# Kernel optimization log

Hardware: AMD Instinct MI355X
Metric: run time of the kernel (lower is better)

Reference implementation:

```python
import jax, jax.numpy as jnp
import numpy as np

N_NODES = 100000


def _gcn_norm(src, dst, n_nodes, n_edges):
    # PyG gcn_norm with add_self_loops=False: deg over target (col) index
    ones = jnp.ones((n_edges,), dtype=jnp.float32)
    deg = jax.ops.segment_sum(ones, dst, num_segments=n_nodes)
    dinv = jnp.where(deg > 0, jax.lax.rsqrt(deg), 0.0)
    return dinv[src] * dinv[dst]  # [E]


def _arma_conv(x, src, dst, ew, init_w, root_w, bias, n_nodes):
    # x: [N, Fin]; init_w/root_w: [K, Fin, Fout]; bias: [K, 1, Fout]
    h = jnp.einsum('nf,kfo->kno', x, init_w)          # [K, N, Fout]
    msg = h[:, src, :] * ew[None, :, None]             # [K, E, Fout]
    agg = jax.vmap(lambda m: jax.ops.segment_sum(m, dst, num_segments=n_nodes))(msg)
    out = agg + jnp.einsum('nf,kfo->kno', x, root_w) + bias
    return jax.nn.relu(out).mean(axis=0)               # mean over stacks K


def setup_inputs() -> dict:
    key = jax.random.key(0)
    ks = jax.random.split(key, 8)
    n, e = N_NODES, 3200000
    nfeat, hid, nclass, K = 512, 16, 40, 2
    x = jax.random.normal(ks[0], (n, nfeat), dtype=jnp.float32)
    edge_index = jax.random.randint(ks[1], (2, e), 0, n, dtype=jnp.int32)
    s1 = (1.0 / np.sqrt(nfeat)).astype(np.float32) if isinstance(np.sqrt(nfeat), np.ndarray) else np.float32(1.0 / np.sqrt(nfeat))
    s2 = np.float32(1.0 / np.sqrt(hid))
    iw1 = jax.random.normal(ks[2], (K, nfeat, hid), dtype=jnp.float32) * s1
    rw1 = jax.random.normal(ks[3], (K, nfeat, hid), dtype=jnp.float32) * s1
    b1 = jax.random.normal(ks[4], (K, 1, hid), dtype=jnp.float32) * 0.01
    iw2 = jax.random.normal(ks[5], (K, hid, nclass), dtype=jnp.float32) * s2
    rw2 = jax.random.normal(ks[6], (K, hid, nclass), dtype=jnp.float32) * s2
    b2 = jax.random.normal(ks[7], (K, 1, nclass), dtype=jnp.float32) * 0.01
    return {'x': x, 'edge_index': edge_index, 'iw1': iw1, 'rw1': rw1, 'b1': b1,
            'iw2': iw2, 'rw2': rw2, 'b2': b2}


def reference(x, edge_index, iw1, rw1, b1, iw2, rw2, b2):
    src, dst = edge_index[0], edge_index[1]
    n = N_NODES
    ew = _gcn_norm(src, dst, n, src.shape[0])
    h = _arma_conv(x, src, dst, ew, iw1, rw1, b1, n)   # [N, 16]
    out = _arma_conv(h, src, dst, ew, iw2, rw2, b2, n) # [N, nclass]
    return out
```

## Files before the change

### kernel.cpp

```cpp
#include <hip/hip_runtime.h>


#define TB 256
#define CHA 4096

typedef __attribute__((ext_vector_type(8))) short bf8;
typedef __attribute__((ext_vector_type(4))) float f4;

__device__ inline unsigned short f2bf_rne(float f) {
  unsigned int u = __float_as_uint(f);
  unsigned int r = u + 0x7fffu + ((u >> 16) & 1u);
  return (unsigned short)(r >> 16);
}
__device__ inline float bf2f(unsigned short h) {
  return __uint_as_float(((unsigned int)h) << 16);
}
__device__ inline float bflo(unsigned int u) { return __uint_as_float(u << 16); }
__device__ inline float bfhi(unsigned int u) { return __uint_as_float(u & 0xffff0000u); }
__device__ inline unsigned int bfpack(float lo, float hi) {
  return (unsigned int)f2bf_rne(lo) | ((unsigned int)f2bf_rne(hi) << 16);
}

#define ACC8(v)                                   \
  do {                                            \
    a[0] += bflo((v).x); a[1] += bfhi((v).x);     \
    a[2] += bflo((v).y); a[3] += bfhi((v).y);     \
    a[4] += bflo((v).z); a[5] += bfhi((v).z);     \
    a[6] += bflo((v).w); a[7] += bfhi((v).w);     \
  } while (0)

#define ACC4(v)                                   \
  do {                                            \
    a[0] += bflo((v).x); a[1] += bfhi((v).x);     \
    a[2] += bflo((v).y); a[3] += bfhi((v).y);     \
  } while (0)

__global__ __launch_bounds__(TB) void k_countA(const int* __restrict__ dst,
                                               int* __restrict__ ccnt, int E) {
  __shared__ int cnt[256];
  int tid = threadIdx.x;
  cnt[tid] = 0;
  __syncthreads();
  int e0 = blockIdx.x * CHA;
  int e1 = min(e0 + CHA, E);
  for (int e = e0 + tid; e < e1; e += TB) atomicAdd(&cnt[dst[e] >> 9], 1);
  __syncthreads();
  if (cnt[tid] > 0) atomicAdd(&ccnt[tid], cnt[tid]);
}

__global__ __launch_bounds__(256) void k_scanC(const int* __restrict__ ccnt,
                                               int* __restrict__ cbase,
                                               int* __restrict__ ccur) {
  __shared__ int sh[256];
  int tid = threadIdx.x;
  int v = ccnt[tid];
  sh[tid] = v;
  __syncthreads();
  for (int d = 1; d < 256; d <<= 1) {
    int t = (tid >= d) ? sh[tid - d] : 0;
    __syncthreads();
    sh[tid] += t;
    __syncthreads();
  }
  int excl = sh[tid] - v;
  cbase[tid] = excl;
  ccur[tid] = excl;
  if (tid == 255) cbase[256] = sh[255];
}

__global__ __launch_bounds__(TB) void k_binA(const int* __restrict__ src,
                                             const int* __restrict__ dst,
                                             int* __restrict__ ccur,
                                             unsigned int* __restrict__ epairs,
                                             int E) {
  __shared__ int cnt[256];
  __shared__ int gb[256];
  int tid = threadIdx.x;
  cnt[tid] = 0;
  __syncthreads();
  int e0 = blockIdx.x * CHA;
  int e1 = min(e0 + CHA, E);
  for (int e = e0 + tid; e < e1; e += TB) atomicAdd(&cnt[dst[e] >> 9], 1);
  __syncthreads();
  int c = cnt[tid];
  if (c > 0) gb[tid] = atomicAdd(&ccur[tid], c);
  __syncthreads();
  cnt[tid] = 0;
  __syncthreads();
  for (int e = e0 + tid; e < e1; e += TB) {
    int dv = dst[e];
    int b = dv >> 9;
    int r = atomicAdd(&cnt[b], 1);
    epairs[gb[b] + r] = ((unsigned int)src[e] << 9) | (unsigned int)(dv & 511);
  }
}

__global__ __launch_bounds__(TB) void k_binB(const unsigned int* __restrict__ epairs,
                                             const int* __restrict__ cbase,
                                             int* __restrict__ degi,
                                             int* __restrict__ offsets,
                                             int* __restrict__ srcs,
                                             float* __restrict__ dinv, int N) {
  __shared__ int cnt[512];
  __shared__ int pre[512];
  int b = blockIdx.x;
  int n0 = b << 9;
  int tid = threadIdx.x;
  int beg = cbase[b], end = cbase[b + 1];
  int i0 = tid, i1 = tid + 256;
  cnt[i0] = 0; cnt[i1] = 0;
  __syncthreads();
  for (int e = beg + tid; e < end; e += TB)
    atomicAdd(&cnt[epairs[e] & 511u], 1);
  __syncthreads();
  pre[i0] = cnt[i0]; pre[i1] = cnt[i1];
  __syncthreads();
  for (int d = 1; d < 512; d <<= 1) {
    int t0 = (i0 >= d) ? pre[i0 - d] : 0;
    int t1 = (i1 >= d) ? pre[i1 - d] : 0;
    __syncthreads();
    pre[i0] += t0; pre[i1] += t1;
    __syncthreads();
  }
  int e0 = pre[i0] - cnt[i0];
  int e1x = pre[i1] - cnt[i1];
  if (n0 + i0 < N) {
    int c0 = cnt[i0];
    degi[n0 + i0] = c0;
    offsets[n0 + i0] = beg + e0;
    dinv[n0 + i0] = c0 > 0 ? rsqrtf((float)c0) : 0.0f;
  }
  if (n0 + i1 < N) {
    int c1 = cnt[i1];
    degi[n0 + i1] = c1;
    offsets[n0 + i1] = beg + e1x;
    dinv[n0 + i1] = c1 > 0 ? rsqrtf((float)c1) : 0.0f;
  }
  __syncthreads();
  cnt[i0] = e0; cnt[i1] = e1x;
  __syncthreads();
  for (int e = beg + tid; e < end; e += TB) {
    unsigned int p = epairs[e];
    int pos = atomicAdd(&cnt[p & 511u], 1);
    srcs[beg + pos] = (int)(p >> 9);
  }
}

__global__ __launch_bounds__(TB) void k_wsplit(const float* __restrict__ iw1,
                                               const float* __restrict__ rw1,
                                               short* __restrict__ Whi,
                                               short* __restrict__ Wlo) {
  int idx = blockIdx.x * TB + threadIdx.x;
  if (idx >= 32768) return;
  int j = idx & 7;
  int l = (idx >> 3) & 63;
  int t = (idx >> 9) & 3;
  int c = idx >> 11;
  int k = c * 32 + (l >> 4) * 8 + j;
  int n = t * 16 + (l & 15);
  float w;
  if (n < 16)
    w = iw1[k * 16 + n];
  else if (n < 32)
    w = iw1[8192 + k * 16 + (n - 16)];
  else if (n < 48)
    w = rw1[k * 16 + (n - 32)];
  else
    w = rw1[8192 + k * 16 + (n - 48)];
  unsigned short h = f2bf_rne(w);
  float res = w - bf2f(h);
  Whi[idx] = (short)h;
  Wlo[idx] = (short)f2bf_rne(res);
}

__global__ __launch_bounds__(TB) void k_gemm1_mfma(const float* __restrict__ x,
                                                   const short* __restrict__ Whi,
                                                   const short* __restrict__ Wlo,
                                                   const float* __restrict__ dinv,
                                                   unsigned short* __restrict__ Hs,
                                                   float* __restrict__ R, int N) {
  int lane = threadIdx.x & 63;
  int wave = threadIdx.x >> 6;
  int row0 = blockIdx.x * 64 + wave * 16;
  int m = lane & 15, quad = lane >> 4;
  int r = row0 + m;
  bool rv = (r < N);
  const float* xr = x + (size_t)r * 512;

  f4 acc[4];
#pragma unroll
  for (int t = 0; t < 4; t++) acc[t] = (f4){0.f, 0.f, 0.f, 0.f};

  for (int c = 0; c < 16; ++c) {
    float xv[8];
    if (rv) {
      f4 a0 = *(const f4*)(xr + c * 32 + quad * 8);
      f4 a1 = *(const f4*)(xr + c * 32 + quad * 8 + 4);
      xv[0] = a0.x; xv[1] = a0.y; xv[2] = a0.z; xv[3] = a0.w;
      xv[4] = a1.x; xv[5] = a1.y; xv[6] = a1.z; xv[7] = a1.w;
    } else {
#pragma unroll
      for (int j = 0; j < 8; ++j) xv[j] = 0.f;
    }
    bf8 ahi, alo;
#pragma unroll
    for (int j = 0; j < 8; ++j) {
      unsigned short h = f2bf_rne(xv[j]);
      float res = xv[j] - bf2f(h);
      ahi[j] = (short)h;
      alo[j] = (short)f2bf_rne(res);
    }
    const short* wb = Whi + ((size_t)(c * 4) * 64 + lane) * 8;
    const short* wl = Wlo + ((size_t)(c * 4) * 64 + lane) * 8;
#pragma unroll
    for (int t = 0; t < 4; ++t) {
      bf8 bh = *(const bf8*)(wb + t * 512);
      bf8 bl = *(const bf8*)(wl + t * 512);
      acc[t] = __builtin_amdgcn_mfma_f32_16x16x32_bf16(ahi, bh, acc[t], 0, 0, 0);
      acc[t] = __builtin_amdgcn_mfma_f32_16x16x32_bf16(alo, bh, acc[t], 0, 0, 0);
      acc[t] = __builtin_amdgcn_mfma_f32_16x16x32_bf16(ahi, bl, acc[t], 0, 0, 0);
    }
  }
  float dv[4];
#pragma unroll
  for (int g = 0; g < 4; ++g) {
    int ro = row0 + quad * 4 + g;
    dv[g] = (ro < N) ? dinv[ro] : 0.f;
  }
#pragma unroll
  for (int t = 0; t < 4; ++t) {
#pragma unroll
    for (int g = 0; g < 4; ++g) {
      int ro = row0 + quad * 4 + g;
      if (ro < N) {
        if (t < 2)
          Hs[(size_t)ro * 32 + t * 16 + m] = f2bf_rne(acc[t][g] * dv[g]);
        else
          R[(size_t)ro * 32 + (t - 2) * 16 + m] = acc[t][g];
      }
    }
  }
}

__global__ __launch_bounds__(TB) void k_prop1(const int* __restrict__ offsets,
                                              const int* __restrict__ degi,
                                              const int* __restrict__ srcs,
                                              const unsigned short* __restrict__ Hs,
                                              const float* __restrict__ R,
                                              const float* __restrict__ dinv,
                                              const float* __restrict__ b1,
                                              float* __restrict__ h,
                                              unsigned short* __restrict__ hs, int N) {
  int tid = blockIdx.x * TB + threadIdx.x;
  int q = tid & 3;
  int n = tid >> 2;
  if (n >= N) return;
  int beg = offsets[n], cnt = degi[n];
  const unsigned short* Hq = Hs + q * 8;
  float a[8];
#pragma unroll
  for (int j = 0; j < 8; j++) a[j] = 0.f;

  int i = 0;
  if (cnt >= 4) {
    int s0 = srcs[beg], s1 = srcs[beg + 1], s2 = srcs[beg + 2], s3 = srcs[beg + 3];
    for (; i + 8 <= cnt; i += 4) {
      uint4 v0 = *(const uint4*)(Hq + (size_t)s0 * 32);
      uint4 v1 = *(const uint4*)(Hq + (size_t)s1 * 32);
      uint4 v2 = *(const uint4*)(Hq + (size_t)s2 * 32);
      uint4 v3 = *(const uint4*)(Hq + (size_t)s3 * 32);
      s0 = srcs[beg + i + 4]; s1 = srcs[beg + i + 5];
      s2 = srcs[beg + i + 6]; s3 = srcs[beg + i + 7];
      ACC8(v0); ACC8(v1); ACC8(v2); ACC8(v3);
    }
    {
      uint4 v0 = *(const uint4*)(Hq + (size_t)s0 * 32);
      uint4 v1 = *(const uint4*)(Hq + (size_t)s1 * 32);
      uint4 v2 = *(const uint4*)(Hq + (size_t)s2 * 32);
      uint4 v3 = *(const uint4*)(Hq + (size_t)s3 * 32);
      ACC8(v0); ACC8(v1); ACC8(v2); ACC8(v3);
      i += 4;
    }
  }
  for (; i < cnt; ++i) {
    int s = srcs[beg + i];
    uint4 v = *(const uint4*)(Hq + (size_t)s * 32);
    ACC8(v);
  }

  float dvn = dinv[n];
  f4 r0 = *(const f4*)(R + (size_t)n * 32 + q * 8);
  f4 r1 = *(const f4*)(R + (size_t)n * 32 + q * 8 + 4);
  float rr[8] = {r0.x, r0.y, r0.z, r0.w, r1.x, r1.y, r1.z, r1.w};
  float vv[8];
#pragma unroll
  for (int j = 0; j < 8; j++) {
    int f = q * 8 + j;
    vv[j] = fmaxf(a[j] * dvn + rr[j] + b1[(f >> 4) * 16 + (f & 15)], 0.f);
  }
  float pv[8];
#pragma unroll
  for (int j = 0; j < 8; j++) pv[j] = __shfl_xor(vv[j], 2);
  if (q < 2) {
    float hv[8];
#pragma unroll
    for (int j = 0; j < 8; j++) hv[j] = 0.5f * (vv[j] + pv[j]);
    f4 o0 = {hv[0], hv[1], hv[2], hv[3]};
    f4 o1 = {hv[4], hv[5], hv[6], hv[7]};
    *(f4*)(h + (size_t)n * 16 + q * 8) = o0;
    *(f4*)(h + (size_t)n * 16 + q * 8 + 4) = o1;
    uint4 ob;
    ob.x = bfpack(hv[0] * dvn, hv[1] * dvn);
    ob.y = bfpack(hv[2] * dvn, hv[3] * dvn);
    ob.z = bfpack(hv[4] * dvn, hv[5] * dvn);
    ob.w = bfpack(hv[6] * dvn, hv[7] * dvn);
    *(uint4*)(hs + (size_t)n * 16 + q * 8) = ob;
  }
}

__global__ __launch_bounds__(TB) void k_prop2(const int* __restrict__ offsets,
                                              const int* __restrict__ degi,
                                              const int* __restrict__ srcs,
                                              const unsigned short* __restrict__ hs,
                                              const float* __restrict__ dinv,
                                              float* __restrict__ Ah, int N) {
  int tid = blockIdx.x * TB + threadIdx.x;
  int q = tid & 3;
  int n = tid >> 2;
  if (n >= N) return;
  int beg = offsets[n], cnt = degi[n];
  const unsigned short* Hq = hs + q * 4;
  float a[4] = {0.f, 0.f, 0.f, 0.f};

  int i = 0;
  if (cnt >= 4) {
    int s0 = srcs[beg], s1 = srcs[beg + 1], s2 = srcs[beg + 2], s3 = srcs[beg + 3];
    for (; i + 8 <= cnt; i += 4) {
      uint2 v0 = *(const uint2*)(Hq + (size_t)s0 * 16);
      uint2 v1 = *(const uint2*)(Hq + (size_t)s1 * 16);
      uint2 v2 = *(const uint2*)(Hq + (size_t)s2 * 16);
      uint2 v3 = *(const uint2*)(Hq + (size_t)s3 * 16);
      s0 = srcs[beg + i + 4]; s1 = srcs[beg + i + 5];
      s2 = srcs[beg + i + 6]; s3 = srcs[beg + i + 7];
      ACC4(v0); ACC4(v1); ACC4(v2); ACC4(v3);
    }
    {
      uint2 v0 = *(const uint2*)(Hq + (size_t)s0 * 16);
      uint2 v1 = *(const uint2*)(Hq + (size_t)s1 * 16);
      uint2 v2 = *(const uint2*)(Hq + (size_t)s2 * 16);
      uint2 v3 = *(const uint2*)(Hq + (size_t)s3 * 16);
      ACC4(v0); ACC4(v1); ACC4(v2); ACC4(v3);
      i += 4;
    }
  }
  for (; i < cnt; ++i) {
    int s = srcs[beg + i];
    uint2 v = *(const uint2*)(Hq + (size_t)s * 16);
    ACC4(v);
  }

  float dvn = dinv[n];
  f4 o = {a[0] * dvn, a[1] * dvn, a[2] * dvn, a[3] * dvn};
  *(f4*)(Ah + (size_t)n * 16 + q * 4) = o;
}

__global__ __launch_bounds__(TB) void k_final(const float* __restrict__ Ah,
                                              const float* __restrict__ h,
                                              const float* __restrict__ iw2,
                                              const float* __restrict__ rw2,
                                              const float* __restrict__ b2,
                                              float* __restrict__ out, int N) {
  __shared__ float w_iw[2 * 16 * 40];
  __shared__ float w_rw[2 * 16 * 40];
  __shared__ float w_b[2 * 40];
  for (int i = threadIdx.x; i < 1280; i += TB) {
    w_iw[i] = iw2[i];
    w_rw[i] = rw2[i];
  }
  for (int i = threadIdx.x; i < 80; i += TB) w_b[i] = b2[i];
  __syncthreads();

  int idx = blockIdx.x * TB + threadIdx.x;
  if (idx >= N * 40) return;
  int n = idx / 40;
  int o = idx - n * 40;
  float a[16], hr[16];
#pragma unroll
  for (int f = 0; f < 16; f++) {
    a[f] = Ah[(size_t)n * 16 + f];
    hr[f] = h[(size_t)n * 16 + f];
  }
  float res = 0.f;
#pragma unroll
  for (int k = 0; k < 2; k++) {
    float s = w_b[k * 40 + o];
#pragma unroll
    for (int f = 0; f < 16; f++) {
      s += a[f] * w_iw[(k * 16 + f) * 40 + o];
      s += hr[f] * w_rw[(k * 16 + f) * 40 + o];
    }
    res += fmaxf(s, 0.f);
  }
  out[idx] = 0.5f * res;
}

extern "C" void kernel_launch(void* const* d_in, const int* in_sizes, int n_in,
                              void* d_out, int out_size, void* d_ws, size_t ws_size,
                              hipStream_t stream) {
  const float* x = (const float*)d_in[0];
  const int* ei = (const int*)d_in[1];
  const float* iw1 = (const float*)d_in[2];
  const float* rw1 = (const float*)d_in[3];
  const float* b1 = (const float*)d_in[4];
  const float* iw2 = (const float*)d_in[5];
  const float* rw2 = (const float*)d_in[6];
  const float* b2 = (const float*)d_in[7];
  float* out = (float*)d_out;

  const int N = in_sizes[0] / 512;
  const int E = in_sizes[1] / 2;
  const int* src = ei;
  const int* dst = ei + E;
  const int NC = (N + 511) >> 9;

  char* base = (char*)d_ws;
  size_t off = 0;
  auto alloc = [&](size_t bytes) -> void* {
    off = (off + 255) & ~(size_t)255;
    void* p = base + off;
    off += bytes;
    return p;
  };
  int* degi = (int*)alloc((size_t)N * 4);
  float* dinv = (float*)alloc((size_t)N * 4);
  int* offsets = (int*)alloc((size_t)N * 4);
  int* ccnt = (int*)alloc(260 * 4);
  int* cbase = (int*)alloc(260 * 4);
  int* ccur = (int*)alloc(260 * 4);
  size_t epair_bytes = (size_t)E * 4;
  size_t r_bytes = (size_t)N * 32 * 4;
  unsigned int* epairs =
      (unsigned int*)alloc(epair_bytes > r_bytes ? epair_bytes : r_bytes);
  int* srcs = (int*)alloc((size_t)E * 4);
  unsigned short* Hs = (unsigned short*)alloc((size_t)N * 32 * 2);
  float* hbuf = (float*)alloc((size_t)N * 16 * 4);
  unsigned short* hs = (unsigned short*)alloc((size_t)N * 16 * 2);
  float* Ah = (float*)alloc((size_t)N * 16 * 4);
  short* Whi = (short*)alloc(32768 * 2);
  short* Wlo = (short*)alloc(32768 * 2);
  float* R = (float*)epairs;
  (void)ws_size;

  hipMemsetAsync(ccnt, 0, 260 * 4, stream);

  int NBLK = (E + CHA - 1) / CHA;
  k_countA<<<NBLK, TB, 0, stream>>>(dst, ccnt, E);
  k_scanC<<<1, 256, 0, stream>>>(ccnt, cbase, ccur);
  k_binA<<<NBLK, TB, 0, stream>>>(src, dst, ccur, epairs, E);
  k_binB<<<NC, TB, 0, stream>>>(epairs, cbase, degi, offsets, srcs, dinv, N);
  k_wsplit<<<128, TB, 0, stream>>>(iw1, rw1, Whi, Wlo);
  k_gemm1_mfma<<<(N + 63) / 64, TB, 0, stream>>>(x, Whi, Wlo, dinv, Hs, R, N);
  k_prop1<<<((size_t)N * 4 + TB - 1) / TB, TB, 0, stream>>>(offsets, degi, srcs, Hs, R,
                                                            dinv, b1, hbuf, hs, N);
  k_prop2<<<((size_t)N * 4 + TB - 1) / TB, TB, 0, stream>>>(offsets, degi, srcs, hs,
                                                            dinv, Ah, N);
  k_final<<<((size_t)N * 40 + TB - 1) / TB, TB, 0, stream>>>(Ah, hbuf, iw2, rw2, b2, out, N);
}
```

Measured before the change: 565.9 us.

## Pad CSR rows to multiples of four and degree-sort nodes for propagation

Each node's CSR neighbor list is padded to a multiple of four entries. The padding points at a zeroed dummy row N, which lets both propagation kernels drop their scalar tail loop. A degree histogram, scan and scatter build a permutation so that threads in a wavefront handle nodes of similar degree, which is meant to reduce divergence in the gather loops. The cost is three extra small kernels, extra padded srcs storage, an indirection through perm, and scattered output writes in prop1 and prop2.

```diff
diff --git a/kernel.cpp b/kernel.cpp
--- a/kernel.cpp
+++ b/kernel.cpp
@@ -3,6 +3,7 @@
 
 #define TB 256
 #define CHA 4096
+#define PADB 1536
 
 typedef __attribute__((ext_vector_type(8))) short bf8;
 typedef __attribute__((ext_vector_type(4))) float f4;
@@ -107,13 +108,16 @@
   int n0 = b << 9;
   int tid = threadIdx.x;
   int beg = cbase[b], end = cbase[b + 1];
+  int pbase = beg + b * PADB;
   int i0 = tid, i1 = tid + 256;
   cnt[i0] = 0; cnt[i1] = 0;
   __syncthreads();
   for (int e = beg + tid; e < end; e += TB)
     atomicAdd(&cnt[epairs[e] & 511u], 1);
   __syncthreads();
-  pre[i0] = cnt[i0]; pre[i1] = cnt[i1];
+  int pd0 = (cnt[i0] + 3) & ~3;
+  int pd1 = (cnt[i1] + 3) & ~3;
+  pre[i0] = pd0; pre[i1] = pd1;
   __syncthreads();
   for (int d = 1; d < 512; d <<= 1) {
     int t0 = (i0 >= d) ? pre[i0 - d] : 0;
@@ -122,36 +126,68 @@
     pre[i0] += t0; pre[i1] += t1;
     __syncthreads();
   }
-  int e0 = pre[i0] - cnt[i0];
-  int e1x = pre[i1] - cnt[i1];
+  int s0 = pre[i0] - pd0;
+  int s1 = pre[i1] - pd1;
   if (n0 + i0 < N) {
     int c0 = cnt[i0];
     degi[n0 + i0] = c0;
-    offsets[n0 + i0] = beg + e0;
+    offsets[n0 + i0] = pbase + s0;
     dinv[n0 + i0] = c0 > 0 ? rsqrtf((float)c0) : 0.0f;
   }
   if (n0 + i1 < N) {
     int c1 = cnt[i1];
     degi[n0 + i1] = c1;
-    offsets[n0 + i1] = beg + e1x;
+    offsets[n0 + i1] = pbase + s1;
     dinv[n0 + i1] = c1 > 0 ? rsqrtf((float)c1) : 0.0f;
   }
   __syncthreads();
-  cnt[i0] = e0; cnt[i1] = e1x;
+  cnt[i0] = s0; cnt[i1] = s1;
   __syncthreads();
   for (int e = beg + tid; e < end; e += TB) {
     unsigned int p = epairs[e];
     int pos = atomicAdd(&cnt[p & 511u], 1);
-    srcs[beg + pos] = (int)(p >> 9);
-  }
+    srcs[pbase + pos] = (int)(p >> 9);
+  }
+  __syncthreads();
+  for (int j = cnt[i0]; j < pre[i0]; ++j) srcs[pbase + j] = N;
+  for (int j = cnt[i1]; j < pre[i1]; ++j) srcs[pbase + j] = N;
+}
+
+__global__ __launch_bounds__(TB) void k_dhist(const int* __restrict__ degi,
+                                              int* __restrict__ dhist, int N) {
+  __shared__ int cnt[256];
+  cnt[threadIdx.x] = 0;
+  __syncthreads();
+  int n = blockIdx.x * TB + threadIdx.x;
+  if (n < N) {
+    int bin = min((degi[n] + 3) >> 2, 255);
+    atomicAdd(&cnt[bin], 1);
+  }
+  __syncthreads();
+  if (cnt[threadIdx.x] > 0) atomicAdd(&dhist[threadIdx.x], cnt[threadIdx.x]);
+}
+
+__global__ __launch_bounds__(TB) void k_dscatter(const int* __restrict__ degi,
+                                                 int* __restrict__ dcur,
+                                                 int* __restrict__ perm, int N) {
+  int n = blockIdx.x * TB + threadIdx.x;
+  if (n >= N) return;
+  int bin = min((degi[n] + 3) >> 2, 255);
+  int pos = atomicAdd(&dcur[bin], 1);
+  perm[pos] = n;
 }
 
 __global__ __launch_bounds__(TB) void k_wsplit(const float* __restrict__ iw1,
                                                const float* __restrict__ rw1,
                                                short* __restrict__ Whi,
-                                               short* __restrict__ Wlo) {
+                                               short* __restrict__ Wlo,
+                                               unsigned short* __restrict__ Hs,
+                                               unsigned short* __restrict__ hs,
+                                               int N) {
   int idx = blockIdx.x * TB + threadIdx.x;
   if (idx >= 32768) return;
+  if (idx < 32) Hs[(size_t)N * 32 + idx] = 0;
+  if (idx < 16) hs[(size_t)N * 16 + idx] = 0;
   int j = idx & 7;
   int l = (idx >> 3) & 63;
   int t = (idx >> 9) & 3;
@@ -242,7 +278,8 @@
   }
 }
 
-__global__ __launch_bounds__(TB) void k_prop1(const int* __restrict__ offsets,
+__global__ __launch_bounds__(TB) void k_prop1(const int* __restrict__ perm,
+                                              const int* __restrict__ offsets,
                                               const int* __restrict__ degi,
                                               const int* __restrict__ srcs,
                                               const unsigned short* __restrict__ Hs,
@@ -253,18 +290,20 @@
                                               unsigned short* __restrict__ hs, int N) {
   int tid = blockIdx.x * TB + threadIdx.x;
   int q = tid & 3;
-  int n = tid >> 2;
-  if (n >= N) return;
+  int idx = tid >> 2;
+  if (idx >= N) return;
+  int n = perm[idx];
   int beg = offsets[n], cnt = degi[n];
+  int pdeg = (cnt + 3) & ~3;
   const unsigned short* Hq = Hs + q * 8;
   float a[8];
 #pragma unroll
   for (int j = 0; j < 8; j++) a[j] = 0.f;
 
-  int i = 0;
-  if (cnt >= 4) {
+  if (pdeg) {
     int s0 = srcs[beg], s1 = srcs[beg + 1], s2 = srcs[beg + 2], s3 = srcs[beg + 3];
-    for (; i + 8 <= cnt; i += 4) {
+    int i = 0;
+    for (; i + 8 <= pdeg; i += 4) {
       uint4 v0 = *(const uint4*)(Hq + (size_t)s0 * 32);
       uint4 v1 = *(const uint4*)(Hq + (size_t)s1 * 32);
       uint4 v2 = *(const uint4*)(Hq + (size_t)s2 * 32);
@@ -279,13 +318,7 @@
       uint4 v2 = *(const uint4*)(Hq + (size_t)s2 * 32);
       uint4 v3 = *(const uint4*)(Hq + (size_t)s3 * 32);
       ACC8(v0); ACC8(v1); ACC8(v2); ACC8(v3);
-      i += 4;
-    }
-  }
-  for (; i < cnt; ++i) {
-    int s = srcs[beg + i];
-    uint4 v = *(const uint4*)(Hq + (size_t)s * 32);
-    ACC8(v);
+    }
   }
 
   float dvn = dinv[n];
@@ -296,7 +329,7 @@
 #pragma unroll
   for (int j = 0; j < 8; j++) {
     int f = q * 8 + j;
-    vv[j] = fmaxf(a[j] * dvn + rr[j] + b1[(f >> 4) * 16 + (f & 15)], 0.f);
+    vv[j] = fmaxf(a[j] * dvn + rr[j] + b1[f], 0.f);
   }
   float pv[8];
 #pragma unroll
@@ -318,7 +351,8 @@
   }
 }
 
-__global__ __launch_bounds__(TB) void k_prop2(const int* __restrict__ offsets,
+__global__ __launch_bounds__(TB) void k_prop2(const int* __restrict__ perm,
+                                              const int* __restrict__ offsets,
                                               const int* __restrict__ degi,
                                               const int* __restrict__ srcs,
                                               const unsigned short* __restrict__ hs,
@@ -326,16 +360,18 @@
                                               float* __restrict__ Ah, int N) {
   int tid = blockIdx.x * TB + threadIdx.x;
   int q = tid & 3;
-  int n = tid >> 2;
-  if (n >= N) return;
+  int idx = tid >> 2;
+  if (idx >= N) return;
+  int n = perm[idx];
   int beg = offsets[n], cnt = degi[n];
+  int pdeg = (cnt + 3) & ~3;
   const unsigned short* Hq = hs + q * 4;
   float a[4] = {0.f, 0.f, 0.f, 0.f};
 
-  int i = 0;
-  if (cnt >= 4) {
+  if (pdeg) {
     int s0 = srcs[beg], s1 = srcs[beg + 1], s2 = srcs[beg + 2], s3 = srcs[beg + 3];
-    for (; i + 8 <= cnt; i += 4) {
+    int i = 0;
+    for (; i + 8 <= pdeg; i += 4) {
       uint2 v0 = *(const uint2*)(Hq + (size_t)s0 * 16);
       uint2 v1 = *(const uint2*)(Hq + (size_t)s1 * 16);
       uint2 v2 = *(const uint2*)(Hq + (size_t)s2 * 16);
@@ -350,13 +386,7 @@
       uint2 v2 = *(const uint2*)(Hq + (size_t)s2 * 16);
       uint2 v3 = *(const uint2*)(Hq + (size_t)s3 * 16);
       ACC4(v0); ACC4(v1); ACC4(v2); ACC4(v3);
-      i += 4;
-    }
-  }
-  for (; i < cnt; ++i) {
-    int s = srcs[beg + i];
-    uint2 v = *(const uint2*)(Hq + (size_t)s * 16);
-    ACC4(v);
+    }
   }
 
   float dvn = dinv[n];
@@ -434,35 +464,44 @@
   int* degi = (int*)alloc((size_t)N * 4);
   float* dinv = (float*)alloc((size_t)N * 4);
   int* offsets = (int*)alloc((size_t)N * 4);
-  int* ccnt = (int*)alloc(260 * 4);
+  int* perm = (int*)alloc((size_t)N * 4);
+  int* cz = (int*)alloc(1040 * 4);
+  int* ccnt = cz;
+  int* dhist = cz + 260;
   int* cbase = (int*)alloc(260 * 4);
   int* ccur = (int*)alloc(260 * 4);
+  int* dbase = (int*)alloc(260 * 4);
+  int* dcur = (int*)alloc(260 * 4);
   size_t epair_bytes = (size_t)E * 4;
   size_t r_bytes = (size_t)N * 32 * 4;
   unsigned int* epairs =
       (unsigned int*)alloc(epair_bytes > r_bytes ? epair_bytes : r_bytes);
-  int* srcs = (int*)alloc((size_t)E * 4);
-  unsigned short* Hs = (unsigned short*)alloc((size_t)N * 32 * 2);
+  int* srcs = (int*)alloc(((size_t)E + 256 * PADB) * 4);
+  unsigned short* Hs = (unsigned short*)alloc((size_t)(N + 1) * 32 * 2);
   float* hbuf = (float*)alloc((size_t)N * 16 * 4);
-  unsigned short* hs = (unsigned short*)alloc((size_t)N * 16 * 2);
+  unsigned short* hs = (unsigned short*)alloc((size_t)(N + 1) * 16 * 2);
   float* Ah = (float*)alloc((size_t)N * 16 * 4);
   short* Whi = (short*)alloc(32768 * 2);
   short* Wlo = (short*)alloc(32768 * 2);
   float* R = (float*)epairs;
   (void)ws_size;
 
-  hipMemsetAsync(ccnt, 0, 260 * 4, stream);
+  hipMemsetAsync(cz, 0, 1040 * 4, stream);
 
   int NBLK = (E + CHA - 1) / CHA;
+  int NNB = (N + TB - 1) / TB;
   k_countA<<<NBLK, TB, 0, stream>>>(dst, ccnt, E);
   k_scanC<<<1, 256, 0, stream>>>(ccnt, cbase, ccur);
   k_binA<<<NBLK, TB, 0, stream>>>(src, dst, ccur, epairs, E);
   k_binB<<<NC, TB, 0, stream>>>(epairs, cbase, degi, offsets, srcs, dinv, N);
-  k_wsplit<<<128, TB, 0, stream>>>(iw1, rw1, Whi, Wlo);
+  k_dhist<<<NNB, TB, 0, stream>>>(degi, dhist, N);
+  k_scanC<<<1, 256, 0, stream>>>(dhist, dbase, dcur);
+  k_dscatter<<<NNB, TB, 0, stream>>>(degi, dcur, perm, N);
+  k_wsplit<<<128, TB, 0, stream>>>(iw1, rw1, Whi, Wlo, Hs, hs, N);
   k_gemm1_mfma<<<(N + 63) / 64, TB, 0, stream>>>(x, Whi, Wlo, dinv, Hs, R, N);
-  k_prop1<<<((size_t)N * 4 + TB - 1) / TB, TB, 0, stream>>>(offsets, degi, srcs, Hs, R,
-                                                            dinv, b1, hbuf, hs, N);
-  k_prop2<<<((size_t)N * 4 + TB - 1) / TB, TB, 0, stream>>>(offsets, degi, srcs, hs,
-                                                            dinv, Ah, N);
+  k_prop1<<<((size_t)N * 4 + TB - 1) / TB, TB, 0, stream>>>(perm, offsets, degi, srcs,
+                                                            Hs, R, dinv, b1, hbuf, hs, N);
+  k_prop2<<<((size_t)N * 4 + TB - 1) / TB, TB, 0, stream>>>(perm, offsets, degi, srcs,
+                                                            hs, dinv, Ah, N);
   k_final<<<((size_t)N * 40 + TB - 1) / TB, TB, 0, stream>>>(Ah, hbuf, iw2, rw2, b2, out, N);
 }
```

Result: slower. 1.059 ms (+87.2%).

## Build CSR via global atomic ranks and pad rows to multiples of four

Applied to the files above, without the earlier changes.

Replaces the two-level bucketed binning (count, scan, bin by chunk, then per-bucket sort) with a per-edge global atomicAdd on degree that records each edge's rank, a three-kernel prefix scan over nodes, and a direct scatter of sources into CSR slots. Each node's edge list is padded to a multiple of four, with the padding pointing at a zeroed sentinel row, so the propagation kernels can drop their scalar tail loops. The cost is contended global atomics on 3.2M edges, extra rank storage and scattered writes, plus dummy gathers for the padding slots. The b1 indexing is also simplified to an equivalent form.

```diff
diff --git a/kernel.cpp b/kernel.cpp
--- a/kernel.cpp
+++ b/kernel.cpp
@@ -2,7 +2,6 @@
 
 
 #define TB 256
-#define CHA 4096
 
 typedef __attribute__((ext_vector_type(8))) short bf8;
 typedef __attribute__((ext_vector_type(4))) float f4;
@@ -35,123 +34,90 @@
     a[2] += bflo((v).y); a[3] += bfhi((v).y);     \
   } while (0)
 
-__global__ __launch_bounds__(TB) void k_countA(const int* __restrict__ dst,
-                                               int* __restrict__ ccnt, int E) {
-  __shared__ int cnt[256];
-  int tid = threadIdx.x;
-  cnt[tid] = 0;
+__global__ __launch_bounds__(TB) void k_deg(const int* __restrict__ dst,
+                                            int* __restrict__ degi,
+                                            int* __restrict__ rank, int E) {
+  int e = blockIdx.x * TB + threadIdx.x;
+  if (e >= E) return;
+  int d = dst[e];
+  rank[e] = atomicAdd(&degi[d], 1);
+}
+
+__global__ __launch_bounds__(TB) void k_scan1(const int* __restrict__ degi,
+                                              int* __restrict__ offsets,
+                                              int* __restrict__ bsum,
+                                              float* __restrict__ dinv, int N) {
+  __shared__ int sh[TB];
+  int t = threadIdx.x;
+  int n = blockIdx.x * TB + t;
+  int d = (n < N) ? degi[n] : 0;
+  int pd = (d + 3) & ~3;
+  sh[t] = pd;
   __syncthreads();
-  int e0 = blockIdx.x * CHA;
-  int e1 = min(e0 + CHA, E);
-  for (int e = e0 + tid; e < e1; e += TB) atomicAdd(&cnt[dst[e] >> 9], 1);
+  for (int o = 1; o < TB; o <<= 1) {
+    int v = (t >= o) ? sh[t - o] : 0;
+    __syncthreads();
+    sh[t] += v;
+    __syncthreads();
+  }
+  if (n < N) {
+    offsets[n] = sh[t] - pd;
+    dinv[n] = d > 0 ? rsqrtf((float)d) : 0.0f;
+  }
+  if (t == TB - 1) bsum[blockIdx.x] = sh[t];
+}
+
+__global__ __launch_bounds__(512) void k_scan2(const int* __restrict__ bsum,
+                                               int* __restrict__ bbase, int NB) {
+  __shared__ int sh[512];
+  int t = threadIdx.x;
+  int v = (t < NB) ? bsum[t] : 0;
+  sh[t] = v;
   __syncthreads();
-  if (cnt[tid] > 0) atomicAdd(&ccnt[tid], cnt[tid]);
-}
-
-__global__ __launch_bounds__(256) void k_scanC(const int* __restrict__ ccnt,
-                                               int* __restrict__ cbase,
-                                               int* __restrict__ ccur) {
-  __shared__ int sh[256];
-  int tid = threadIdx.x;
-  int v = ccnt[tid];
-  sh[tid] = v;
-  __syncthreads();
-  for (int d = 1; d < 256; d <<= 1) {
-    int t = (tid >= d) ? sh[tid - d] : 0;
+  for (int o = 1; o < 512; o <<= 1) {
+    int x = (t >= o) ? sh[t - o] : 0;
     __syncthreads();
-    sh[tid] += t;
+    sh[t] += x;
     __syncthreads();
   }
-  int excl = sh[tid] - v;
-  cbase[tid] = excl;
-  ccur[tid] = excl;
-  if (tid == 255) cbase[256] = sh[255];
-}
-
-__global__ __launch_bounds__(TB) void k_binA(const int* __restrict__ src,
-                                             const int* __restrict__ dst,
-                                             int* __restrict__ ccur,
-                                             unsigned int* __restrict__ epairs,
-                                             int E) {
-  __shared__ int cnt[256];
-  __shared__ int gb[256];
-  int tid = threadIdx.x;
-  cnt[tid] = 0;
-  __syncthreads();
-  int e0 = blockIdx.x * CHA;
-  int e1 = min(e0 + CHA, E);
-  for (int e = e0 + tid; e < e1; e += TB) atomicAdd(&cnt[dst[e] >> 9], 1);
-  __syncthreads();
-  int c = cnt[tid];
-  if (c > 0) gb[tid] = atomicAdd(&ccur[tid], c);
-  __syncthreads();
-  cnt[tid] = 0;
-  __syncthreads();
-  for (int e = e0 + tid; e < e1; e += TB) {
-    int dv = dst[e];
-    int b = dv >> 9;
-    int r = atomicAdd(&cnt[b], 1);
-    epairs[gb[b] + r] = ((unsigned int)src[e] << 9) | (unsigned int)(dv & 511);
-  }
-}
-
-__global__ __launch_bounds__(TB) void k_binB(const unsigned int* __restrict__ epairs,
-                                             const int* __restrict__ cbase,
-                                             int* __restrict__ degi,
-                                             int* __restrict__ offsets,
-                                             int* __restrict__ srcs,
-                                             float* __restrict__ dinv, int N) {
-  __shared__ int cnt[512];
-  __shared__ int pre[512];
-  int b = blockIdx.x;
-  int n0 = b << 9;
-  int tid = threadIdx.x;
-  int beg = cbase[b], end = cbase[b + 1];
-  int i0 = tid, i1 = tid + 256;
-  cnt[i0] = 0; cnt[i1] = 0;
-  __syncthreads();
-  for (int e = beg + tid; e < end; e += TB)
-    atomicAdd(&cnt[epairs[e] & 511u], 1);
-  __syncthreads();
-  pre[i0] = cnt[i0]; pre[i1] = cnt[i1];
-  __syncthreads();
-  for (int d = 1; d < 512; d <<= 1) {
-    int t0 = (i0 >= d) ? pre[i0 - d] : 0;
-    int t1 = (i1 >= d) ? pre[i1 - d] : 0;
-    __syncthreads();
-    pre[i0] += t0; pre[i1] += t1;
-    __syncthreads();
-  }
-  int e0 = pre[i0] - cnt[i0];
-  int e1x = pre[i1] - cnt[i1];
-  if (n0 + i0 < N) {
-    int c0 = cnt[i0];
-    degi[n0 + i0] = c0;
-    offsets[n0 + i0] = beg + e0;
-    dinv[n0 + i0] = c0 > 0 ? rsqrtf((float)c0) : 0.0f;
-  }
-  if (n0 + i1 < N) {
-    int c1 = cnt[i1];
-    degi[n0 + i1] = c1;
-    offsets[n0 + i1] = beg + e1x;
-    dinv[n0 + i1] = c1 > 0 ? rsqrtf((float)c1) : 0.0f;
-  }
-  __syncthreads();
-  cnt[i0] = e0; cnt[i1] = e1x;
-  __syncthreads();
-  for (int e = beg + tid; e < end; e += TB) {
-    unsigned int p = epairs[e];
-    int pos = atomicAdd(&cnt[p & 511u], 1);
-    srcs[beg + pos] = (int)(p >> 9);
-  }
+  if (t < NB) bbase[t] = sh[t] - v;
+}
+
+__global__ __launch_bounds__(TB) void k_scan3(const int* __restrict__ degi,
+                                              int* __restrict__ offsets,
+                                              const int* __restrict__ bbase,
+                                              int* __restrict__ srcs, int N) {
+  int n = blockIdx.x * TB + threadIdx.x;
+  if (n >= N) return;
+  int off = offsets[n] + bbase[n >> 8];
+  offsets[n] = off;
+  int d = degi[n];
+  int pd = (d + 3) & ~3;
+  for (int j = d; j < pd; ++j) srcs[off + j] = N;
+}
+
+__global__ __launch_bounds__(TB) void k_scatter(const int* __restrict__ src,
+                                                const int* __restrict__ dst,
+                                                const int* __restrict__ rank,
+                                                const int* __restrict__ offsets,
+                                                int* __restrict__ srcs, int E) {
+  int e = blockIdx.x * TB + threadIdx.x;
+  if (e >= E) return;
+  int d = dst[e];
+  srcs[offsets[d] + rank[e]] = src[e];
 }
 
 __global__ __launch_bounds__(TB) void k_wsplit(const float* __restrict__ iw1,
                                                const float* __restrict__ rw1,
                                                short* __restrict__ Whi,
-                                               short* __restrict__ Wlo) {
+                                               short* __restrict__ Wlo,
+                                               unsigned short* __restrict__ Hs,
+                                               unsigned short* __restrict__ hs,
+                                               int N) {
   int idx = blockIdx.x * TB + threadIdx.x;
   if (idx >= 32768) return;
+  if (idx < 32) Hs[(size_t)N * 32 + idx] = 0;
+  if (idx < 16) hs[(size_t)N * 16 + idx] = 0;
   int j = idx & 7;
   int l = (idx >> 3) & 63;
   int t = (idx >> 9) & 3;
@@ -256,15 +222,16 @@
   int n = tid >> 2;
   if (n >= N) return;
   int beg = offsets[n], cnt = degi[n];
+  int pdeg = (cnt + 3) & ~3;
   const unsigned short* Hq = Hs + q * 8;
   float a[8];
 #pragma unroll
   for (int j = 0; j < 8; j++) a[j] = 0.f;
 
-  int i = 0;
-  if (cnt >= 4) {
+  if (pdeg) {
     int s0 = srcs[beg], s1 = srcs[beg + 1], s2 = srcs[beg + 2], s3 = srcs[beg + 3];
-    for (; i + 8 <= cnt; i += 4) {
+    int i = 0;
+    for (; i + 8 <= pdeg; i += 4) {
       uint4 v0 = *(const uint4*)(Hq + (size_t)s0 * 32);
       uint4 v1 = *(const uint4*)(Hq + (size_t)s1 * 32);
       uint4 v2 = *(const uint4*)(Hq + (size_t)s2 * 32);
@@ -279,13 +246,7 @@
       uint4 v2 = *(const uint4*)(Hq + (size_t)s2 * 32);
       uint4 v3 = *(const uint4*)(Hq + (size_t)s3 * 32);
       ACC8(v0); ACC8(v1); ACC8(v2); ACC8(v3);
-      i += 4;
-    }
-  }
-  for (; i < cnt; ++i) {
-    int s = srcs[beg + i];
-    uint4 v = *(const uint4*)(Hq + (size_t)s * 32);
-    ACC8(v);
+    }
   }
 
   float dvn = dinv[n];
@@ -296,7 +257,7 @@
 #pragma unroll
   for (int j = 0; j < 8; j++) {
     int f = q * 8 + j;
-    vv[j] = fmaxf(a[j] * dvn + rr[j] + b1[(f >> 4) * 16 + (f & 15)], 0.f);
+    vv[j] = fmaxf(a[j] * dvn + rr[j] + b1[f], 0.f);
   }
   float pv[8];
 #pragma unroll
@@ -329,13 +290,14 @@
   int n = tid >> 2;
   if (n >= N) return;
   int beg = offsets[n], cnt = degi[n];
+  int pdeg = (cnt + 3) & ~3;
   const unsigned short* Hq = hs + q * 4;
   float a[4] = {0.f, 0.f, 0.f, 0.f};
 
-  int i = 0;
-  if (cnt >= 4) {
+  if (pdeg) {
     int s0 = srcs[beg], s1 = srcs[beg + 1], s2 = srcs[beg + 2], s3 = srcs[beg + 3];
-    for (; i + 8 <= cnt; i += 4) {
+    int i = 0;
+    for (; i + 8 <= pdeg; i += 4) {
       uint2 v0 = *(const uint2*)(Hq + (size_t)s0 * 16);
       uint2 v1 = *(const uint2*)(Hq + (size_t)s1 * 16);
       uint2 v2 = *(const uint2*)(Hq + (size_t)s2 * 16);
@@ -350,13 +312,7 @@
       uint2 v2 = *(const uint2*)(Hq + (size_t)s2 * 16);
       uint2 v3 = *(const uint2*)(Hq + (size_t)s3 * 16);
       ACC4(v0); ACC4(v1); ACC4(v2); ACC4(v3);
-      i += 4;
-    }
-  }
-  for (; i < cnt; ++i) {
-    int s = srcs[beg + i];
-    uint2 v = *(const uint2*)(Hq + (size_t)s * 16);
-    ACC4(v);
+    }
   }
 
   float dvn = dinv[n];
@@ -421,7 +377,6 @@
   const int E = in_sizes[1] / 2;
   const int* src = ei;
   const int* dst = ei + E;
-  const int NC = (N + 511) >> 9;
 
   char* base = (char*)d_ws;
   size_t off = 0;
@@ -434,35 +389,34 @@
   int* degi = (int*)alloc((size_t)N * 4);
   float* dinv = (float*)alloc((size_t)N * 4);
   int* offsets = (int*)alloc((size_t)N * 4);
-  int* ccnt = (int*)alloc(260 * 4);
-  int* cbase = (int*)alloc(260 * 4);
-  int* ccur = (int*)alloc(260 * 4);
-  size_t epair_bytes = (size_t)E * 4;
+  int* bsum = (int*)alloc(512 * 4);
+  int* bbase = (int*)alloc(512 * 4);
+  size_t rank_bytes = (size_t)E * 4;
   size_t r_bytes = (size_t)N * 32 * 4;
-  unsigned int* epairs =
-      (unsigned int*)alloc(epair_bytes > r_bytes ? epair_bytes : r_bytes);
-  int* srcs = (int*)alloc((size_t)E * 4);
-  unsigned short* Hs = (unsigned short*)alloc((size_t)N * 32 * 2);
+  int* rank = (int*)alloc(rank_bytes > r_bytes ? rank_bytes : r_bytes);
+  int* srcs = (int*)alloc(((size_t)E + 4 * (size_t)N) * 4);
+  unsigned short* Hs = (unsigned short*)alloc((size_t)(N + 1) * 32 * 2);
   float* hbuf = (float*)alloc((size_t)N * 16 * 4);
-  unsigned short* hs = (unsigned short*)alloc((size_t)N * 16 * 2);
+  unsigned short* hs = (unsigned short*)alloc((size_t)(N + 1) * 16 * 2);
   float* Ah = (float*)alloc((size_t)N * 16 * 4);
   short* Whi = (short*)alloc(32768 * 2);
   short* Wlo = (short*)alloc(32768 * 2);
-  float* R = (float*)epairs;
+  float* R = (float*)rank;
   (void)ws_size;
 
-  hipMemsetAsync(ccnt, 0, 260 * 4, stream);
-
-  int NBLK = (E + CHA - 1) / CHA;
-  k_countA<<<NBLK, TB, 0, stream>>>(dst, ccnt, E);
-  k_scanC<<<1, 256, 0, stream>>>(ccnt, cbase, ccur);
-  k_binA<<<NBLK, TB, 0, stream>>>(src, dst, ccur, epairs, E);
-  k_binB<<<NC, TB, 0, stream>>>(epairs, cbase, degi, offsets, srcs, dinv, N);
-  k_wsplit<<<128, TB, 0, stream>>>(iw1, rw1, Whi, Wlo);
+  hipMemsetAsync(degi, 0, (size_t)N * 4, stream);
+
+  int EB = (E + TB - 1) / TB;
+  int NB1 = (N + TB - 1) / TB;
+  k_deg<<<EB, TB, 0, stream>>>(dst, degi, rank, E);
+  k_scan1<<<NB1, TB, 0, stream>>>(degi, offsets, bsum, dinv, N);
+  k_scan2<<<1, 512, 0, stream>>>(bsum, bbase, NB1);
+  k_scan3<<<NB1, TB, 0, stream>>>(degi, offsets, bbase, srcs, N);
+  k_scatter<<<EB, TB, 0, stream>>>(src, dst, rank, offsets, srcs, E);
+  k_wsplit<<<128, TB, 0, stream>>>(iw1, rw1, Whi, Wlo, Hs, hs, N);
   k_gemm1_mfma<<<(N + 63) / 64, TB, 0, stream>>>(x, Whi, Wlo, dinv, Hs, R, N);
-  k_prop1<<<((size_t)N * 4 + TB - 1) / TB, TB, 0, stream>>>(offsets, degi, srcs, Hs, R,
-                                                            dinv, b1, hbuf, hs, N);
-  k_prop2<<<((size_t)N * 4 + TB - 1) / TB, TB, 0, stream>>>(offsets, degi, srcs, hs,
-                                                            dinv, Ah, N);
+  int PG = ((size_t)N * 4 + TB - 1) / TB;
+  k_prop1<<<PG, TB, 0, stream>>>(offsets, degi, srcs, Hs, R, dinv, b1, hbuf, hs, N);
+  k_prop2<<<PG, TB, 0, stream>>>(offsets, degi, srcs, hs, dinv, Ah, N);
   k_final<<<((size_t)N * 40 + TB - 1) / TB, TB, 0, stream>>>(Ah, hbuf, iw2, rw2, b2, out, N);
 }
```

Result: slower. 655.3 us (+15.8%).

## Use fixed-capacity buckets and pad CSR rows to multiples of eight

Applied to the files above, without the earlier changes.

The separate count and scan passes over the destination indices are replaced by fixed-capacity bucket regions. Capacity is sized from the mean bucket load plus slack, so one full read of dst and two launches go away. Each node's neighbour list is also padded to a multiple of 8 with a dummy source that points at an extra zero feature row. This lets both propagation kernels load indices as int4 and run an 8-wide unrolled gather with no scalar tail loop. The trade-offs are extra wasted gathers for the padding and a risk of bucket overflow on skewed degree distributions, since overflow is not checked.

```diff
diff --git a/kernel.cpp b/kernel.cpp
--- a/kernel.cpp
+++ b/kernel.cpp
@@ -35,37 +35,8 @@
     a[2] += bflo((v).y); a[3] += bfhi((v).y);     \
   } while (0)
 
-__global__ __launch_bounds__(TB) void k_countA(const int* __restrict__ dst,
-                                               int* __restrict__ ccnt, int E) {
-  __shared__ int cnt[256];
-  int tid = threadIdx.x;
-  cnt[tid] = 0;
-  __syncthreads();
-  int e0 = blockIdx.x * CHA;
-  int e1 = min(e0 + CHA, E);
-  for (int e = e0 + tid; e < e1; e += TB) atomicAdd(&cnt[dst[e] >> 9], 1);
-  __syncthreads();
-  if (cnt[tid] > 0) atomicAdd(&ccnt[tid], cnt[tid]);
-}
-
-__global__ __launch_bounds__(256) void k_scanC(const int* __restrict__ ccnt,
-                                               int* __restrict__ cbase,
-                                               int* __restrict__ ccur) {
-  __shared__ int sh[256];
-  int tid = threadIdx.x;
-  int v = ccnt[tid];
-  sh[tid] = v;
-  __syncthreads();
-  for (int d = 1; d < 256; d <<= 1) {
-    int t = (tid >= d) ? sh[tid - d] : 0;
-    __syncthreads();
-    sh[tid] += t;
-    __syncthreads();
-  }
-  int excl = sh[tid] - v;
-  cbase[tid] = excl;
-  ccur[tid] = excl;
-  if (tid == 255) cbase[256] = sh[255];
+__global__ __launch_bounds__(256) void k_init(int* __restrict__ ccur, int cap) {
+  ccur[threadIdx.x] = threadIdx.x * cap;
 }
 
 __global__ __launch_bounds__(TB) void k_binA(const int* __restrict__ src,
@@ -96,24 +67,29 @@
 }
 
 __global__ __launch_bounds__(TB) void k_binB(const unsigned int* __restrict__ epairs,
-                                             const int* __restrict__ cbase,
+                                             const int* __restrict__ ccur,
                                              int* __restrict__ degi,
                                              int* __restrict__ offsets,
                                              int* __restrict__ srcs,
-                                             float* __restrict__ dinv, int N) {
+                                             float* __restrict__ dinv,
+                                             int N, int cap, int scap) {
   __shared__ int cnt[512];
   __shared__ int pre[512];
   int b = blockIdx.x;
   int n0 = b << 9;
   int tid = threadIdx.x;
-  int beg = cbase[b], end = cbase[b + 1];
+  int beg = b * cap;
+  int end = ccur[b];
+  int pbase = b * scap;
   int i0 = tid, i1 = tid + 256;
   cnt[i0] = 0; cnt[i1] = 0;
   __syncthreads();
   for (int e = beg + tid; e < end; e += TB)
     atomicAdd(&cnt[epairs[e] & 511u], 1);
   __syncthreads();
-  pre[i0] = cnt[i0]; pre[i1] = cnt[i1];
+  int pd0 = (cnt[i0] + 7) & ~7;
+  int pd1 = (cnt[i1] + 7) & ~7;
+  pre[i0] = pd0; pre[i1] = pd1;
   __syncthreads();
   for (int d = 1; d < 512; d <<= 1) {
     int t0 = (i0 >= d) ? pre[i0 - d] : 0;
@@ -122,36 +98,44 @@
     pre[i0] += t0; pre[i1] += t1;
     __syncthreads();
   }
-  int e0 = pre[i0] - cnt[i0];
-  int e1x = pre[i1] - cnt[i1];
+  int s0 = pre[i0] - pd0;
+  int s1 = pre[i1] - pd1;
   if (n0 + i0 < N) {
     int c0 = cnt[i0];
     degi[n0 + i0] = c0;
-    offsets[n0 + i0] = beg + e0;
+    offsets[n0 + i0] = pbase + s0;
     dinv[n0 + i0] = c0 > 0 ? rsqrtf((float)c0) : 0.0f;
   }
   if (n0 + i1 < N) {
     int c1 = cnt[i1];
     degi[n0 + i1] = c1;
-    offsets[n0 + i1] = beg + e1x;
+    offsets[n0 + i1] = pbase + s1;
     dinv[n0 + i1] = c1 > 0 ? rsqrtf((float)c1) : 0.0f;
   }
   __syncthreads();
-  cnt[i0] = e0; cnt[i1] = e1x;
+  cnt[i0] = s0; cnt[i1] = s1;
   __syncthreads();
   for (int e = beg + tid; e < end; e += TB) {
     unsigned int p = epairs[e];
     int pos = atomicAdd(&cnt[p & 511u], 1);
-    srcs[beg + pos] = (int)(p >> 9);
-  }
+    srcs[pbase + pos] = (int)(p >> 9);
+  }
+  __syncthreads();
+  for (int j = cnt[i0]; j < pre[i0]; ++j) srcs[pbase + j] = N;
+  for (int j = cnt[i1]; j < pre[i1]; ++j) srcs[pbase + j] = N;
 }
 
 __global__ __launch_bounds__(TB) void k_wsplit(const float* __restrict__ iw1,
                                                const float* __restrict__ rw1,
                                                short* __restrict__ Whi,
-                                               short* __restrict__ Wlo) {
+                                               short* __restrict__ Wlo,
+                                               unsigned short* __restrict__ Hs,
+                                               unsigned short* __restrict__ hs,
+                                               int N) {
   int idx = blockIdx.x * TB + threadIdx.x;
   if (idx >= 32768) return;
+  if (idx < 32) Hs[(size_t)N * 32 + idx] = 0;
+  if (idx < 16) hs[(size_t)N * 16 + idx] = 0;
   int j = idx & 7;
   int l = (idx >> 3) & 63;
   int t = (idx >> 9) & 3;
@@ -256,36 +240,42 @@
   int n = tid >> 2;
   if (n >= N) return;
   int beg = offsets[n], cnt = degi[n];
+  int pdeg = (cnt + 7) & ~7;
   const unsigned short* Hq = Hs + q * 8;
   float a[8];
 #pragma unroll
   for (int j = 0; j < 8; j++) a[j] = 0.f;
 
-  int i = 0;
-  if (cnt >= 4) {
-    int s0 = srcs[beg], s1 = srcs[beg + 1], s2 = srcs[beg + 2], s3 = srcs[beg + 3];
-    for (; i + 8 <= cnt; i += 4) {
-      uint4 v0 = *(const uint4*)(Hq + (size_t)s0 * 32);
-      uint4 v1 = *(const uint4*)(Hq + (size_t)s1 * 32);
-      uint4 v2 = *(const uint4*)(Hq + (size_t)s2 * 32);
-      uint4 v3 = *(const uint4*)(Hq + (size_t)s3 * 32);
-      s0 = srcs[beg + i + 4]; s1 = srcs[beg + i + 5];
-      s2 = srcs[beg + i + 6]; s3 = srcs[beg + i + 7];
+  if (pdeg) {
+    int4 sa = *(const int4*)(srcs + beg);
+    int4 sb = *(const int4*)(srcs + beg + 4);
+    int i = 0;
+    for (; i + 16 <= pdeg; i += 8) {
+      uint4 v0 = *(const uint4*)(Hq + (size_t)sa.x * 32);
+      uint4 v1 = *(const uint4*)(Hq + (size_t)sa.y * 32);
+      uint4 v2 = *(const uint4*)(Hq + (size_t)sa.z * 32);
+      uint4 v3 = *(const uint4*)(Hq + (size_t)sa.w * 32);
+      uint4 v4 = *(const uint4*)(Hq + (size_t)sb.x * 32);
+      uint4 v5 = *(const uint4*)(Hq + (size_t)sb.y * 32);
+      uint4 v6 = *(const uint4*)(Hq + (size_t)sb.z * 32);
+      uint4 v7 = *(const uint4*)(Hq + (size_t)sb.w * 32);
+      sa = *(const int4*)(srcs + beg + i + 8);
+      sb = *(const int4*)(srcs + beg + i + 12);
       ACC8(v0); ACC8(v1); ACC8(v2); ACC8(v3);
+      ACC8(v4); ACC8(v5); ACC8(v6); ACC8(v7);
     }
     {
-      uint4 v0 = *(const uint4*)(Hq + (size_t)s0 * 32);
-      uint4 v1 = *(const uint4*)(Hq + (size_t)s1 * 32);
-      uint4 v2 = *(const uint4*)(Hq + (size_t)s2 * 32);
-      uint4 v3 = *(const uint4*)(Hq + (size_t)s3 * 32);
+      uint4 v0 = *(const uint4*)(Hq + (size_t)sa.x * 32);
+      uint4 v1 = *(const uint4*)(Hq + (size_t)sa.y * 32);
+      uint4 v2 = *(const uint4*)(Hq + (size_t)sa.z * 32);
+      uint4 v3 = *(const uint4*)(Hq + (size_t)sa.w * 32);
+      uint4 v4 = *(const uint4*)(Hq + (size_t)sb.x * 32);
+      uint4 v5 = *(const uint4*)(Hq + (size_t)sb.y * 32);
+      uint4 v6 = *(const uint4*)(Hq + (size_t)sb.z * 32);
+      uint4 v7 = *(const uint4*)(Hq + (size_t)sb.w * 32);
       ACC8(v0); ACC8(v1); ACC8(v2); ACC8(v3);
-      i += 4;
-    }
-  }
-  for (; i < cnt; ++i) {
-    int s = srcs[beg + i];
-    uint4 v = *(const uint4*)(Hq + (size_t)s * 32);
-    ACC8(v);
+      ACC8(v4); ACC8(v5); ACC8(v6); ACC8(v7);
+    }
   }
 
   float dvn = dinv[n];
@@ -296,7 +286,7 @@
 #pragma unroll
   for (int j = 0; j < 8; j++) {
     int f = q * 8 + j;
-    vv[j] = fmaxf(a[j] * dvn + rr[j] + b1[(f >> 4) * 16 + (f & 15)], 0.f);
+    vv[j] = fmaxf(a[j] * dvn + rr[j] + b1[f], 0.f);
   }
   float pv[8];
 #pragma unroll
@@ -329,34 +319,40 @@
   int n = tid >> 2;
   if (n >= N) return;
   int beg = offsets[n], cnt = degi[n];
+  int pdeg = (cnt + 7) & ~7;
   const unsigned short* Hq = hs + q * 4;
   float a[4] = {0.f, 0.f, 0.f, 0.f};
 
-  int i = 0;
-  if (cnt >= 4) {
-    int s0 = srcs[beg], s1 = srcs[beg + 1], s2 = srcs[beg + 2], s3 = srcs[beg + 3];
-    for (; i + 8 <= cnt; i += 4) {
-      uint2 v0 = *(const uint2*)(Hq + (size_t)s0 * 16);
-      uint2 v1 = *(const uint2*)(Hq + (size_t)s1 * 16);
-      uint2 v2 = *(const uint2*)(Hq + (size_t)s2 * 16);
-      uint2 v3 = *(const uint2*)(Hq + (size_t)s3 * 16);
-      s0 = srcs[beg + i + 4]; s1 = srcs[beg + i + 5];
-      s2 = srcs[beg + i + 6]; s3 = srcs[beg + i + 7];
+  if (pdeg) {
+    int4 sa = *(const int4*)(srcs + beg);
+    int4 sb = *(const int4*)(srcs + beg + 4);
+    int i = 0;
+    for (; i + 16 <= pdeg; i += 8) {
+      uint2 v0 = *(const uint2*)(Hq + (size_t)sa.x * 16);
+      uint2 v1 = *(const uint2*)(Hq + (size_t)sa.y * 16);
+      uint2 v2 = *(const uint2*)(Hq + (size_t)sa.z * 16);
+      uint2 v3 = *(const uint2*)(Hq + (size_t)sa.w * 16);
+      uint2 v4 = *(const uint2*)(Hq + (size_t)sb.x * 16);
+      uint2 v5 = *(const uint2*)(Hq + (size_t)sb.y * 16);
+      uint2 v6 = *(const uint2*)(Hq + (size_t)sb.z * 16);
+      uint2 v7 = *(const uint2*)(Hq + (size_t)sb.w * 16);
+      sa = *(const int4*)(srcs + beg + i + 8);
+      sb = *(const int4*)(srcs + beg + i + 12);
       ACC4(v0); ACC4(v1); ACC4(v2); ACC4(v3);
+      ACC4(v4); ACC4(v5); ACC4(v6); ACC4(v7);
     }
     {
-      uint2 v0 = *(const uint2*)(Hq + (size_t)s0 * 16);
-      uint2 v1 = *(const uint2*)(Hq + (size_t)s1 * 16);
-      uint2 v2 = *(const uint2*)(Hq + (size_t)s2 * 16);
-      uint2 v3 = *(const uint2*)(Hq + (size_t)s3 * 16);
+      uint2 v0 = *(const uint2*)(Hq + (size_t)sa.x * 16);
+      uint2 v1 = *(const uint2*)(Hq + (size_t)sa.y * 16);
+      uint2 v2 = *(const uint2*)(Hq + (size_t)sa.z * 16);
+      uint2 v3 = *(const uint2*)(Hq + (size_t)sa.w * 16);
+      uint2 v4 = *(const uint2*)(Hq + (size_t)sb.x * 16);
+      uint2 v5 = *(const uint2*)(Hq + (size_t)sb.y * 16);
+      uint2 v6 = *(const uint2*)(Hq + (size_t)sb.z * 16);
+      uint2 v7 = *(const uint2*)(Hq + (size_t)sb.w * 16);
       ACC4(v0); ACC4(v1); ACC4(v2); ACC4(v3);
-      i += 4;
-    }
-  }
-  for (; i < cnt; ++i) {
-    int s = srcs[beg + i];
-    uint2 v = *(const uint2*)(Hq + (size_t)s * 16);
-    ACC4(v);
+      ACC4(v4); ACC4(v5); ACC4(v6); ACC4(v7);
+    }
   }
 
   float dvn = dinv[n];
@@ -423,6 +419,10 @@
   const int* dst = ei + E;
   const int NC = (N + 511) >> 9;
 
+  int mean = (E + NC - 1) / NC;
+  int cap = (mean + mean / 8 + 256 + 7) & ~7;
+  int scap = cap + 7 * 512;
+
   char* base = (char*)d_ws;
   size_t off = 0;
   auto alloc = [&](size_t bytes) -> void* {
@@ -434,35 +434,29 @@
   int* degi = (int*)alloc((size_t)N * 4);
   float* dinv = (float*)alloc((size_t)N * 4);
   int* offsets = (int*)alloc((size_t)N * 4);
-  int* ccnt = (int*)alloc(260 * 4);
-  int* cbase = (int*)alloc(260 * 4);
-  int* ccur = (int*)alloc(260 * 4);
-  size_t epair_bytes = (size_t)E * 4;
+  int* ccur = (int*)alloc(256 * 4);
+  size_t epair_bytes = (size_t)NC * cap * 4;
   size_t r_bytes = (size_t)N * 32 * 4;
   unsigned int* epairs =
       (unsigned int*)alloc(epair_bytes > r_bytes ? epair_bytes : r_bytes);
-  int* srcs = (int*)alloc((size_t)E * 4);
-  unsigned short* Hs = (unsigned short*)alloc((size_t)N * 32 * 2);
+  int* srcs = (int*)alloc((size_t)NC * scap * 4);
+  unsigned short* Hs = (unsigned short*)alloc((size_t)(N + 1) * 32 * 2);
   float* hbuf = (float*)alloc((size_t)N * 16 * 4);
-  unsigned short* hs = (unsigned short*)alloc((size_t)N * 16 * 2);
+  unsigned short* hs = (unsigned short*)alloc((size_t)(N + 1) * 16 * 2);
   float* Ah = (float*)alloc((size_t)N * 16 * 4);
   short* Whi = (short*)alloc(32768 * 2);
   short* Wlo = (short*)alloc(32768 * 2);
   float* R = (float*)epairs;
   (void)ws_size;
 
-  hipMemsetAsync(ccnt, 0, 260 * 4, stream);
-
   int NBLK = (E + CHA - 1) / CHA;
-  k_countA<<<NBLK, TB, 0, stream>>>(dst, ccnt, E);
-  k_scanC<<<1, 256, 0, stream>>>(ccnt, cbase, ccur);
+  k_init<<<1, 256, 0, stream>>>(ccur, cap);
   k_binA<<<NBLK, TB, 0, stream>>>(src, dst, ccur, epairs, E);
-  k_binB<<<NC, TB, 0, stream>>>(epairs, cbase, degi, offsets, srcs, dinv, N);
-  k_wsplit<<<128, TB, 0, stream>>>(iw1, rw1, Whi, Wlo);
+  k_binB<<<NC, TB, 0, stream>>>(epairs, ccur, degi, offsets, srcs, dinv, N, cap, scap);
+  k_wsplit<<<128, TB, 0, stream>>>(iw1, rw1, Whi, Wlo, Hs, hs, N);
   k_gemm1_mfma<<<(N + 63) / 64, TB, 0, stream>>>(x, Whi, Wlo, dinv, Hs, R, N);
-  k_prop1<<<((size_t)N * 4 + TB - 1) / TB, TB, 0, stream>>>(offsets, degi, srcs, Hs, R,
-                                                            dinv, b1, hbuf, hs, N);
-  k_prop2<<<((size_t)N * 4 + TB - 1) / TB, TB, 0, stream>>>(offsets, degi, srcs, hs,
-                                                            dinv, Ah, N);
+  int PG = ((size_t)N * 4 + TB - 1) / TB;
+  k_prop1<<<PG, TB, 0, stream>>>(offsets, degi, srcs, Hs, R, dinv, b1, hbuf, hs, N);
+  k_prop2<<<PG, TB, 0, stream>>>(offsets, degi, srcs, hs, dinv, Ah, N);
   k_final<<<((size_t)N * 40 + TB - 1) / TB, TB, 0, stream>>>(Ah, hbuf, iw2, rw2, b2, out, N);
 }
```

After: 540.5 us. 4.5% less time.
